# Kernel optimization log

Measured on AMD Instinct MI355X. Metric: run time of the kernel, lower is better.

The kernel has to match this reference:

```python
import jax, jax.numpy as jnp
import numpy as np

WS = 7
C = 384
NH = 12
HD = C // NH
HID = 4 * C


def layernorm(x, g, b, eps=1e-5):
    m = jnp.mean(x, axis=-1, keepdims=True)
    v = jnp.mean((x - m) ** 2, axis=-1, keepdims=True)
    return (x - m) * jax.lax.rsqrt(v + eps) * g + b


def setup_inputs() -> dict:
    key = jax.random.key(0)
    ks = jax.random.split(key, 12)
    s = 0.02
    return {
        "tokens": jax.random.normal(ks[0], (2, 8, 56 * 56, C), jnp.float32),
        "in_proj_w": jax.random.normal(ks[1], (3 * C, C), jnp.float32) * s,
        "in_proj_b": jnp.zeros((3 * C,), jnp.float32),
        "out_w": jax.random.normal(ks[2], (C, C), jnp.float32) * s,
        "out_b": jnp.zeros((C,), jnp.float32),
        "ln1_g": jnp.ones((C,), jnp.float32),
        "ln1_b": jnp.zeros((C,), jnp.float32),
        "w1": jax.random.normal(ks[3], (HID, C), jnp.float32) * s,
        "b1": jnp.zeros((HID,), jnp.float32),
        "w2": jax.random.normal(ks[4], (C, HID), jnp.float32) * s,
        "b2": jnp.zeros((C,), jnp.float32),
        "ln2_g": jnp.ones((C,), jnp.float32),
        "ln2_b": jnp.zeros((C,), jnp.float32),
        "h": 56,
        "w": 56,
    }


def _block(tokens, in_proj_w, in_proj_b, out_w, out_b, ln1_g, ln1_b, w1, b1, w2, b2, ln2_g, ln2_b, h, w):
    b, t, _, c = tokens.shape
    orig_h, orig_w = h, w
    x = tokens.reshape(b, t, h, w, c)
    pad_h = (-h) % WS
    pad_w = (-w) % WS
    if pad_h > 0 or pad_w > 0:
        x = jnp.pad(x, ((0, 0), (0, 0), (0, pad_h), (0, pad_w), (0, 0)))
        h, w = h + pad_h, w + pad_w
    nh, nw = h // WS, w // WS
    # window partition -> [N, 49, C]
    x = x.reshape(b, t, nh, WS, nw, WS, c).transpose(0, 1, 2, 4, 3, 5, 6)
    win = x.reshape(b * t * nh * nw, WS * WS, c)
    # MHA (torch nn.MultiheadAttention semantics)
    a = layernorm(win, ln1_g, ln1_b)
    qkv = a @ in_proj_w.T + in_proj_b  # [N, 49, 3C]
    q, k, v = jnp.split(qkv, 3, axis=-1)
    n, s, _ = q.shape
    q = q.reshape(n, s, NH, HD).transpose(0, 2, 1, 3)
    k = k.reshape(n, s, NH, HD).transpose(0, 2, 1, 3)
    v = v.reshape(n, s, NH, HD).transpose(0, 2, 1, 3)
    scores = jnp.einsum("nhqd,nhkd->nhqk", q, k) / jnp.sqrt(jnp.asarray(HD, q.dtype))
    p = jax.nn.softmax(scores, axis=-1)
    o = jnp.einsum("nhqk,nhkd->nhqd", p, v).transpose(0, 2, 1, 3).reshape(n, s, c)
    win = win + (o @ out_w.T + out_b)
    # MLP
    m = layernorm(win, ln2_g, ln2_b)
    m = jax.nn.gelu(m @ w1.T + b1, approximate=False) @ w2.T + b2
    win = win + m
    # window reverse
    x = win.reshape(b, t, nh, nw, WS, WS, c).transpose(0, 1, 2, 4, 3, 5, 6).reshape(b, t, h, w, c)
    x = x[:, :, :orig_h, :orig_w, :]
    return x.reshape(b, t, orig_h * orig_w, c)


def reference(tokens, in_proj_w, in_proj_b, out_w, out_b, ln1_g, ln1_b, w1, b1, w2, b2, ln2_g, ln2_b, h, w):
    return _block(tokens, in_proj_w, in_proj_b, out_w, out_b, ln1_g, ln1_b, w1, b1, w2, b2, ln2_g, ln2_b, h, w)
```

## Files before the change

### kernel.cpp

```cpp
#include <hip/hip_runtime.h>
#include <hip/hip_bf16.h>
#include <math.h>

using short8 = __attribute__((ext_vector_type(8))) short;
using f32x4  = __attribute__((ext_vector_type(4))) float;

#define MFMA_B16(A,B,C) __builtin_amdgcn_mfma_f32_16x16x32_bf16((A),(B),(C),0,0,0)

#define ALN_STR 392
#define ALN_SZ  38416
#define POOL    76832
#define PS      34816
#define QK_STR  72
#define VT_STR  72
#define OH_STR  72
#define HID_STR 136
#define SMEM_BYTES 146464

__device__ __forceinline__ unsigned short f2bfu(float x) {
  unsigned u = __float_as_uint(x);
  return (unsigned short)((u + 0x7fffu + ((u >> 16) & 1u)) >> 16);
}
__device__ __forceinline__ unsigned pk2(float a, float b) {
  return (unsigned)f2bfu(a) | ((unsigned)f2bfu(b) << 16);
}

template<bool WBF>
__device__ __forceinline__ short8 loadW(const void* base, int tile, int K8, int kcb,
                                        int l, int row, int ldk, int k0) {
  if constexpr (WBF) {
    return *(const short8*)((const unsigned short*)base +
                            (((size_t)(tile * K8 + kcb)) << 7) + l * 8);
  } else {
    const float* p = (const float*)base + (size_t)row * ldk + k0;
    float4 x = *(const float4*)p;
    float4 y = *(const float4*)(p + 4);
    short8 r;
    r[0]=(short)f2bfu(x.x); r[1]=(short)f2bfu(x.y); r[2]=(short)f2bfu(x.z); r[3]=(short)f2bfu(x.w);
    r[4]=(short)f2bfu(y.x); r[5]=(short)f2bfu(y.y); r[6]=(short)f2bfu(y.z); r[7]=(short)f2bfu(y.w);
    return r;
  }
}

__global__ void cvt_pack(const float* __restrict__ src, unsigned short* __restrict__ dst,
                         int K, int n) {
  int K8 = K >> 3;
  int i = blockIdx.x * blockDim.x + threadIdx.x;
  if (i >= n) return;
  int e = i & 7;
  int idx = i >> 3;
  int r = idx & 15; idx >>= 4;
  int kc = idx % K8, ci = idx / K8;
  dst[i] = f2bfu(src[(size_t)(ci * 16 + r) * K + kc * 8 + e]);
}

template<bool WBF>
__global__ __launch_bounds__(1024, 4)
void swin_mfma(const float* __restrict__ tokens,
               const void* __restrict__ ipw,  const float* __restrict__ ipb,
               const void* __restrict__ outw, const float* __restrict__ outb,
               const float* __restrict__ ln1g, const float* __restrict__ ln1b,
               const void* __restrict__ w1,   const float* __restrict__ b1,
               const void* __restrict__ w2,   const float* __restrict__ b2,
               const float* __restrict__ ln2g, const float* __restrict__ ln2b,
               float* __restrict__ out)
{
  extern __shared__ char smem[];
  const int tid = threadIdx.x;
  const int win = tid >> 9;
  const int wv  = (tid >> 6) & 7;
  const int l   = tid & 63;
  const int cl  = l & 15, kg = l >> 4;
  const int wid = blockIdx.x * 2 + win;
  const int iw = wid & 7, ih = (wid >> 3) & 7, bt = wid >> 6;

  unsigned short* aln = (unsigned short*)(smem + win * ALN_SZ);
  char* pool = smem + POOL + win * PS;
  unsigned short* q2   = (unsigned short*)(pool);
  unsigned short* k2   = (unsigned short*)(pool + 7056);
  unsigned short* vT2  = (unsigned short*)(pool + 14112);
  unsigned short* oh   = (unsigned short*)(pool + 23328);
  unsigned short* hid0 = (unsigned short*)(pool);
  unsigned short* hid1 = (unsigned short*)(pool + 17408);

  auto gidx = [&](int r, int c) -> size_t {
    int wi = r / 7, wj = r - wi * 7;
    return ((size_t)bt * 3136 + (size_t)((ih*7 + wi) * 56 + iw*7 + wj)) * 384 + c;
  };

  auto ln_pass = [&](const float* src, const float* gw, const float* gb) {
    int row = (tid >> 3) & 63, lj = tid & 7;
    if (row < 49) {
      size_t base = gidx(row, 0);
      float4 xv[12];
      float sx = 0.f, sxx = 0.f;
      #pragma unroll
      for (int k = 0; k < 12; ++k) {
        xv[k] = *(const float4*)&src[base + (lj + 8*k) * 4];
        sx  += xv[k].x + xv[k].y + xv[k].z + xv[k].w;
        sxx += xv[k].x*xv[k].x + xv[k].y*xv[k].y + xv[k].z*xv[k].z + xv[k].w*xv[k].w;
      }
      #pragma unroll
      for (int d = 1; d < 8; d <<= 1) { sx += __shfl_xor(sx, d, 8); sxx += __shfl_xor(sxx, d, 8); }
      float mean = sx * (1.f/384.f);
      float rs = rsqrtf(sxx * (1.f/384.f) - mean*mean + 1e-5f);
      unsigned short* arow = aln + row * ALN_STR;
      #pragma unroll
      for (int k = 0; k < 12; ++k) {
        int c = (lj + 8*k) * 4;
        float4 gv = *(const float4*)&gw[c];
        float4 bv = *(const float4*)&gb[c];
        unsigned u0 = pk2((xv[k].x-mean)*rs*gv.x + bv.x, (xv[k].y-mean)*rs*gv.y + bv.y);
        unsigned u1 = pk2((xv[k].z-mean)*rs*gv.z + bv.z, (xv[k].w-mean)*rs*gv.w + bv.w);
        *(uint2*)&arow[c] = make_uint2(u0, u1);
      }
    }
  };

  const int ri0 = wv & 3, chalf = wv >> 2;
  const int arow0 = (cl + 16 * ri0) * ALN_STR;

  auto qkv = [&](int pr) {
    #pragma unroll
    for (int half = 0; half < 2; ++half) {
      int tilea[3], growa[3], parta[3], wta[3];
      #pragma unroll
      for (int j = 0; j < 3; ++j) {
        int ci = chalf + 2 * (half * 3 + j);
        parta[j] = ci >> 2; wta[j] = ci & 3;
        tilea[j] = parta[j] * 24 + pr * 4 + wta[j];
        growa[j] = parta[j] * 384 + pr * 64 + wta[j] * 16 + cl;
      }
      f32x4 d0{0,0,0,0}, d1{0,0,0,0}, d2{0,0,0,0};
      short8 a_c  = *(const short8*)&aln[arow0 + kg*8];
      short8 b0_c = loadW<WBF>(ipw, tilea[0], 48, 0, l, growa[0], 384, kg*8);
      short8 b1_c = loadW<WBF>(ipw, tilea[1], 48, 0, l, growa[1], 384, kg*8);
      short8 b2_c = loadW<WBF>(ipw, tilea[2], 48, 0, l, growa[2], 384, kg*8);
      #pragma unroll
      for (int kt = 0; kt < 12; ++kt) {
        short8 a_n, b0_n, b1_n, b2_n;
        if (kt < 11) {
          int k1 = (kt+1)*32 + kg*8;
          a_n  = *(const short8*)&aln[arow0 + k1];
          b0_n = loadW<WBF>(ipw, tilea[0], 48, (kt+1)*4, l, growa[0], 384, k1);
          b1_n = loadW<WBF>(ipw, tilea[1], 48, (kt+1)*4, l, growa[1], 384, k1);
          b2_n = loadW<WBF>(ipw, tilea[2], 48, (kt+1)*4, l, growa[2], 384, k1);
        }
        d0 = MFMA_B16(a_c, b0_c, d0);
        d1 = MFMA_B16(a_c, b1_c, d1);
        d2 = MFMA_B16(a_c, b2_c, d2);
        a_c = a_n; b0_c = b0_n; b1_c = b1_n; b2_c = b2_n;
      }
      #pragma unroll
      for (int j = 0; j < 3; ++j) {
        f32x4 dd = (j == 0) ? d0 : (j == 1) ? d1 : d2;
        int within = wta[j] * 16 + cl;
        float bias = ipb[growa[j]];
        float scl = (parta[j] == 0) ? 0.17677669529663687f : 1.f;
        #pragma unroll
        for (int rg = 0; rg < 4; ++rg) {
          int row = kg * 4 + rg + 16 * ri0;
          if (row < 49) {
            unsigned short bv = f2bfu((dd[rg] + bias) * scl);
            if      (parta[j] == 0) q2[row * QK_STR + within] = bv;
            else if (parta[j] == 1) k2[row * QK_STR + within] = bv;
            else                    vT2[within * VT_STR + row] = bv;
          }
        }
      }
    }
  };

  for (int i = (tid & 511); i < (64*VT_STR)/2; i += 512)
    ((unsigned*)(pool + 14112))[i] = 0u;
  ln_pass(tokens, ln1g, ln1b);
  __syncthreads();

  f32x4 opacc[3][4];
  #pragma unroll
  for (int a = 0; a < 3; ++a)
    #pragma unroll
    for (int b = 0; b < 4; ++b) opacc[a][b] = f32x4{0.f,0.f,0.f,0.f};

  qkv(0);
  __syncthreads();

  const int hl = wv & 1, qci = wv >> 1;

  for (int pr = 0; pr < 6; ++pr) {
    {
      short8 bq = *(const short8*)&q2[(16*qci + cl) * QK_STR + hl*32 + kg*8];
      f32x4 dsc[4];
      #pragma unroll
      for (int kri = 0; kri < 4; ++kri) {
        short8 ak = *(const short8*)&k2[(16*kri + cl) * QK_STR + hl*32 + kg*8];
        f32x4 z{0.f,0.f,0.f,0.f};
        dsc[kri] = MFMA_B16(ak, bq, z);
      }
      float ev[4][4];
      float mx = -1e30f;
      #pragma unroll
      for (int kri = 0; kri < 4; ++kri)
        #pragma unroll
        for (int r = 0; r < 4; ++r) {
          int kidx = 16*kri + 4*kg + r;
          float v = (kidx < 49) ? dsc[kri][r] : -1e30f;
          ev[kri][r] = v;
          mx = fmaxf(mx, v);
        }
      mx = fmaxf(mx, __shfl_xor(mx, 16));
      mx = fmaxf(mx, __shfl_xor(mx, 32));
      float sum = 0.f;
      #pragma unroll
      for (int kri = 0; kri < 4; ++kri)
        #pragma unroll
        for (int r = 0; r < 4; ++r) {
          float e = __expf(ev[kri][r] - mx);
          ev[kri][r] = e; sum += e;
        }
      sum += __shfl_xor(sum, 16);
      sum += __shfl_xor(sum, 32);
      float inv = 1.f / sum;
      unsigned pk[4][2];
      #pragma unroll
      for (int kri = 0; kri < 4; ++kri) {
        pk[kri][0] = pk2(ev[kri][0]*inv, ev[kri][1]*inv);
        pk[kri][1] = pk2(ev[kri][2]*inv, ev[kri][3]*inv);
      }
      f32x4 dot0{0.f,0.f,0.f,0.f}, dot1{0.f,0.f,0.f,0.f};
      const int sA = cl + 32 * (kg & 1);
      const bool hi = (kg >> 1) & 1;
      #pragma unroll
      for (int kt = 0; kt < 2; ++kt) {
        unsigned x0 = (unsigned)__shfl((int)pk[2*kt][0],   sA);
        unsigned x1 = (unsigned)__shfl((int)pk[2*kt][1],   sA);
        unsigned x2 = (unsigned)__shfl((int)pk[2*kt][0],   sA + 16);
        unsigned x3 = (unsigned)__shfl((int)pk[2*kt][1],   sA + 16);
        unsigned y0 = (unsigned)__shfl((int)pk[2*kt+1][0], sA);
        unsigned y1 = (unsigned)__shfl((int)pk[2*kt+1][1], sA);
        unsigned y2 = (unsigned)__shfl((int)pk[2*kt+1][0], sA + 16);
        unsigned y3 = (unsigned)__shfl((int)pk[2*kt+1][1], sA + 16);
        uint4 bu = make_uint4(hi ? y0 : x0, hi ? y1 : x1, hi ? y2 : x2, hi ? y3 : x3);
        short8 bfrag = *(short8*)&bu;
        short8 a0 = *(const short8*)&vT2[(hl*32 +  0 + cl) * VT_STR + kt*32 + kg*8];
        short8 a1 = *(const short8*)&vT2[(hl*32 + 16 + cl) * VT_STR + kt*32 + kg*8];
        dot0 = MFMA_B16(a0, bfrag, dot0);
        dot1 = MFMA_B16(a1, bfrag, dot1);
      }
      int q = 16*qci + cl;
      if (q < 49) {
        int base = q * OH_STR + hl*32 + kg*4;
        *(unsigned*)&oh[base     ] = pk2(dot0[0], dot0[1]);
        *(unsigned*)&oh[base +  2] = pk2(dot0[2], dot0[3]);
        *(unsigned*)&oh[base + 16] = pk2(dot1[0], dot1[1]);
        *(unsigned*)&oh[base + 18] = pk2(dot1[2], dot1[3]);
      }
    }
    __syncthreads();

    {
      short8 ao[4][2];
      #pragma unroll
      for (int ri = 0; ri < 4; ++ri)
        #pragma unroll
        for (int kt = 0; kt < 2; ++kt)
          ao[ri][kt] = *(const short8*)&oh[(cl + 16*ri) * OH_STR + kt*32 + kg*8];
      #pragma unroll
      for (int cii = 0; cii < 3; ++cii) {
        #pragma unroll
        for (int kt = 0; kt < 2; ++kt) {
          short8 bw = loadW<WBF>(outw, wv*3 + cii, 48, pr*8 + kt*4, l,
                                 (wv*3 + cii)*16 + cl, 384, pr*64 + kt*32 + kg*8);
          opacc[cii][0] = MFMA_B16(ao[0][kt], bw, opacc[cii][0]);
          opacc[cii][1] = MFMA_B16(ao[1][kt], bw, opacc[cii][1]);
          opacc[cii][2] = MFMA_B16(ao[2][kt], bw, opacc[cii][2]);
          opacc[cii][3] = MFMA_B16(ao[3][kt], bw, opacc[cii][3]);
        }
      }
      if (pr < 5) qkv(pr + 1);
    }
    __syncthreads();
  }

  #pragma unroll
  for (int cii = 0; cii < 3; ++cii) {
    int col = (wv*3 + cii) * 16 + cl;
    float ob = outb[col];
    #pragma unroll
    for (int ri = 0; ri < 4; ++ri) {
      #pragma unroll
      for (int rg = 0; rg < 4; ++rg) {
        int row = kg*4 + rg + 16*ri;
        if (row < 49) {
          size_t g = gidx(row, col);
          out[g] = tokens[g] + opacc[cii][ri][rg] + ob;
        }
      }
    }
  }
  __syncthreads();

  ln_pass(out, ln2g, ln2b);
  __syncthreads();

  f32x4 macc[3][4];
  #pragma unroll
  for (int a = 0; a < 3; ++a)
    #pragma unroll
    for (int b = 0; b < 4; ++b) macc[a][b] = f32x4{0.f,0.f,0.f,0.f};

  auto mlp1 = [&](int cc, unsigned short* hb) {
    int tile = cc * 8 + wv;
    int n = cc * 128 + wv * 16 + cl;
    f32x4 e0{0,0,0,0}, e1{0,0,0,0}, e2{0,0,0,0}, e3{0,0,0,0};
    short8 bw_c = loadW<WBF>(w1, tile, 48, 0, l, n, 384, kg*8);
    #pragma unroll
    for (int kt = 0; kt < 12; ++kt) {
      short8 bw_n;
      if (kt < 11)
        bw_n = loadW<WBF>(w1, tile, 48, (kt+1)*4, l, n, 384, (kt+1)*32 + kg*8);
      int k0 = kt * 32 + kg * 8;
      short8 a0 = *(const short8*)&aln[(cl     ) * ALN_STR + k0];
      short8 a1 = *(const short8*)&aln[(cl + 16) * ALN_STR + k0];
      short8 a2 = *(const short8*)&aln[(cl + 32) * ALN_STR + k0];
      short8 a3 = *(const short8*)&aln[(cl + 48) * ALN_STR + k0];
      e0 = MFMA_B16(a0, bw_c, e0);
      e1 = MFMA_B16(a1, bw_c, e1);
      e2 = MFMA_B16(a2, bw_c, e2);
      e3 = MFMA_B16(a3, bw_c, e3);
      bw_c = bw_n;
    }
    float bb = b1[n];
    #pragma unroll
    for (int ri = 0; ri < 4; ++ri) {
      f32x4 ee = (ri == 0) ? e0 : (ri == 1) ? e1 : (ri == 2) ? e2 : e3;
      #pragma unroll
      for (int rg = 0; rg < 4; ++rg) {
        int row = kg*4 + rg + 16*ri;
        if (row < 49) {
          float x = ee[rg] + bb;
          float t2 = 0.044715f * x * x;
          float arg = __builtin_fmaf(t2, x, x);
          float e = __expf(1.5957691216f * arg);
          float gl = x * (e / (e + 1.f));
          hb[row * HID_STR + wv*16 + cl] = f2bfu(gl);
        }
      }
    }
  };
  auto mlp2 = [&](int cc, const unsigned short* hb) {
    short8 c0_c = loadW<WBF>(w2, wv*3+0, 192, cc*16, l, (wv*3+0)*16+cl, 1536, cc*128 + kg*8);
    short8 c1_c = loadW<WBF>(w2, wv*3+1, 192, cc*16, l, (wv*3+1)*16+cl, 1536, cc*128 + kg*8);
    short8 c2_c = loadW<WBF>(w2, wv*3+2, 192, cc*16, l, (wv*3+2)*16+cl, 1536, cc*128 + kg*8);
    #pragma unroll
    for (int kt = 0; kt < 4; ++kt) {
      short8 c0_n, c1_n, c2_n;
      if (kt < 3) {
        int kcb = cc*16 + (kt+1)*4, k1 = cc*128 + (kt+1)*32 + kg*8;
        c0_n = loadW<WBF>(w2, wv*3+0, 192, kcb, l, (wv*3+0)*16+cl, 1536, k1);
        c1_n = loadW<WBF>(w2, wv*3+1, 192, kcb, l, (wv*3+1)*16+cl, 1536, k1);
        c2_n = loadW<WBF>(w2, wv*3+2, 192, kcb, l, (wv*3+2)*16+cl, 1536, k1);
      }
      int k0 = kt * 32 + kg * 8;
      short8 h0_ = *(const short8*)&hb[(cl     ) * HID_STR + k0];
      short8 h1_ = *(const short8*)&hb[(cl + 16) * HID_STR + k0];
      short8 h2_ = *(const short8*)&hb[(cl + 32) * HID_STR + k0];
      short8 h3_ = *(const short8*)&hb[(cl + 48) * HID_STR + k0];
      macc[0][0] = MFMA_B16(h0_, c0_c, macc[0][0]);
      macc[0][1] = MFMA_B16(h1_, c0_c, macc[0][1]);
      macc[0][2] = MFMA_B16(h2_, c0_c, macc[0][2]);
      macc[0][3] = MFMA_B16(h3_, c0_c, macc[0][3]);
      macc[1][0] = MFMA_B16(h0_, c1_c, macc[1][0]);
      macc[1][1] = MFMA_B16(h1_, c1_c, macc[1][1]);
      macc[1][2] = MFMA_B16(h2_, c1_c, macc[1][2]);
      macc[1][3] = MFMA_B16(h3_, c1_c, macc[1][3]);
      macc[2][0] = MFMA_B16(h0_, c2_c, macc[2][0]);
      macc[2][1] = MFMA_B16(h1_, c2_c, macc[2][1]);
      macc[2][2] = MFMA_B16(h2_, c2_c, macc[2][2]);
      macc[2][3] = MFMA_B16(h3_, c2_c, macc[2][3]);
      c0_c = c0_n; c1_c = c1_n; c2_c = c2_n;
    }
  };

  mlp1(0, hid0);
  __syncthreads();
  for (int cc = 1; cc < 12; ++cc) {
    mlp2(cc - 1, ((cc - 1) & 1) ? hid1 : hid0);
    mlp1(cc, (cc & 1) ? hid1 : hid0);
    __syncthreads();
  }
  mlp2(11, hid1);

  #pragma unroll
  for (int cii = 0; cii < 3; ++cii) {
    int col = (wv*3 + cii) * 16 + cl;
    float bb2 = b2[col];
    #pragma unroll
    for (int ri = 0; ri < 4; ++ri) {
      #pragma unroll
      for (int rg = 0; rg < 4; ++rg) {
        int row = kg*4 + rg + 16*ri;
        if (row < 49) {
          size_t g = gidx(row, col);
          out[g] = out[g] + macc[cii][ri][rg] + bb2;
        }
      }
    }
  }
}

#define WS_IPW  0
#define WS_OUTW 442368
#define WS_W1   589824
#define WS_W2   1179648
#define WS_TOT  1769472

extern "C" void kernel_launch(void* const* d_in, const int* in_sizes, int n_in,
                              void* d_out, int out_size, void* d_ws, size_t ws_size,
                              hipStream_t stream) {
  (void)in_sizes; (void)n_in; (void)out_size;
  const float* tokens = (const float*)d_in[0];
  const float* ipw  = (const float*)d_in[1];
  const float* ipb  = (const float*)d_in[2];
  const float* outw = (const float*)d_in[3];
  const float* outb = (const float*)d_in[4];
  const float* ln1g = (const float*)d_in[5];
  const float* ln1b = (const float*)d_in[6];
  const float* w1   = (const float*)d_in[7];
  const float* b1   = (const float*)d_in[8];
  const float* w2   = (const float*)d_in[9];
  const float* b2   = (const float*)d_in[10];
  const float* ln2g = (const float*)d_in[11];
  const float* ln2b = (const float*)d_in[12];
  float* out = (float*)d_out;

  bool wbf = (ws_size >= (size_t)WS_TOT * 2);
  if (wbf) {
    unsigned short* wsp = (unsigned short*)d_ws;
    hipLaunchKernelGGL(cvt_pack, dim3((442368+511)/512), dim3(512), 0, stream, ipw,  wsp + WS_IPW,  384,  442368);
    hipLaunchKernelGGL(cvt_pack, dim3((147456+511)/512), dim3(512), 0, stream, outw, wsp + WS_OUTW, 384,  147456);
    hipLaunchKernelGGL(cvt_pack, dim3((589824+511)/512), dim3(512), 0, stream, w1,   wsp + WS_W1,   384,  589824);
    hipLaunchKernelGGL(cvt_pack, dim3((589824+511)/512), dim3(512), 0, stream, w2,   wsp + WS_W2,   1536, 589824);
    (void)hipFuncSetAttribute((const void*)swin_mfma<true>,
                              hipFuncAttributeMaxDynamicSharedMemorySize, SMEM_BYTES);
    hipLaunchKernelGGL((swin_mfma<true>), dim3(512), dim3(1024), SMEM_BYTES, stream,
                       tokens, (const void*)(wsp + WS_IPW), ipb,
                       (const void*)(wsp + WS_OUTW), outb, ln1g, ln1b,
                       (const void*)(wsp + WS_W1), b1, (const void*)(wsp + WS_W2), b2,
                       ln2g, ln2b, out);
  } else {
    (void)hipFuncSetAttribute((const void*)swin_mfma<false>,
                              hipFuncAttributeMaxDynamicSharedMemorySize, SMEM_BYTES);
    hipLaunchKernelGGL((swin_mfma<false>), dim3(512), dim3(1024), SMEM_BYTES, stream,
                       tokens, (const void*)ipw, ipb, (const void*)outw, outb, ln1g, ln1b,
                       (const void*)w1, b1, (const void*)w2, b2, ln2g, ln2b, out);
  }
}
```

Before: 501.2 us.

## Repartition MFMA warp tiling to row-block by column-half for out-proj and MLP

Changes the per-wave work split in the out-projection and both MLP GEMMs. Previously each wave covered all four 16-row blocks for a few output columns; now each wave owns one row block and half of the columns. The LN2 activation fragments for its row block are kept in registers (alnA), which removes repeated LDS reads in MLP1. The manual software prefetch of weights in the QKV and MLP loops is dropped in favour of straight loads. The trade-off is more weight fragment loads per wave, since each wave now loads four times as many distinct weight tiles, and higher register pressure from alnA.

```diff
diff --git a/kernel.cpp b/kernel.cpp
--- a/kernel.cpp
+++ b/kernel.cpp
@@ -117,8 +117,9 @@
     }
   };
 
-  const int ri0 = wv & 3, chalf = wv >> 2;
-  const int arow0 = (cl + 16 * ri0) * ALN_STR;
+  const int ri = wv & 3;
+  const int ch = wv >> 2;
+  const int arow0 = (cl + 16 * ri) * ALN_STR;
 
   auto qkv = [&](int pr) {
     #pragma unroll
@@ -126,30 +127,22 @@
       int tilea[3], growa[3], parta[3], wta[3];
       #pragma unroll
       for (int j = 0; j < 3; ++j) {
-        int ci = chalf + 2 * (half * 3 + j);
+        int ci = ch + 2 * (half * 3 + j);
         parta[j] = ci >> 2; wta[j] = ci & 3;
         tilea[j] = parta[j] * 24 + pr * 4 + wta[j];
         growa[j] = parta[j] * 384 + pr * 64 + wta[j] * 16 + cl;
       }
       f32x4 d0{0,0,0,0}, d1{0,0,0,0}, d2{0,0,0,0};
-      short8 a_c  = *(const short8*)&aln[arow0 + kg*8];
-      short8 b0_c = loadW<WBF>(ipw, tilea[0], 48, 0, l, growa[0], 384, kg*8);
-      short8 b1_c = loadW<WBF>(ipw, tilea[1], 48, 0, l, growa[1], 384, kg*8);
-      short8 b2_c = loadW<WBF>(ipw, tilea[2], 48, 0, l, growa[2], 384, kg*8);
       #pragma unroll
       for (int kt = 0; kt < 12; ++kt) {
-        short8 a_n, b0_n, b1_n, b2_n;
-        if (kt < 11) {
-          int k1 = (kt+1)*32 + kg*8;
-          a_n  = *(const short8*)&aln[arow0 + k1];
-          b0_n = loadW<WBF>(ipw, tilea[0], 48, (kt+1)*4, l, growa[0], 384, k1);
-          b1_n = loadW<WBF>(ipw, tilea[1], 48, (kt+1)*4, l, growa[1], 384, k1);
-          b2_n = loadW<WBF>(ipw, tilea[2], 48, (kt+1)*4, l, growa[2], 384, k1);
-        }
-        d0 = MFMA_B16(a_c, b0_c, d0);
-        d1 = MFMA_B16(a_c, b1_c, d1);
-        d2 = MFMA_B16(a_c, b2_c, d2);
-        a_c = a_n; b0_c = b0_n; b1_c = b1_n; b2_c = b2_n;
+        int k0 = kt * 32 + kg * 8;
+        short8 a  = *(const short8*)&aln[arow0 + k0];
+        short8 b0 = loadW<WBF>(ipw, tilea[0], 48, kt*4, l, growa[0], 384, k0);
+        short8 bb1 = loadW<WBF>(ipw, tilea[1], 48, kt*4, l, growa[1], 384, k0);
+        short8 bb2 = loadW<WBF>(ipw, tilea[2], 48, kt*4, l, growa[2], 384, k0);
+        d0 = MFMA_B16(a, b0, d0);
+        d1 = MFMA_B16(a, bb1, d1);
+        d2 = MFMA_B16(a, bb2, d2);
       }
       #pragma unroll
       for (int j = 0; j < 3; ++j) {
@@ -159,7 +152,7 @@
         float scl = (parta[j] == 0) ? 0.17677669529663687f : 1.f;
         #pragma unroll
         for (int rg = 0; rg < 4; ++rg) {
-          int row = kg * 4 + rg + 16 * ri0;
+          int row = kg * 4 + rg + 16 * ri;
           if (row < 49) {
             unsigned short bv = f2bfu((dd[rg] + bias) * scl);
             if      (parta[j] == 0) q2[row * QK_STR + within] = bv;
@@ -176,11 +169,9 @@
   ln_pass(tokens, ln1g, ln1b);
   __syncthreads();
 
-  f32x4 opacc[3][4];
+  f32x4 opacc[12];
   #pragma unroll
-  for (int a = 0; a < 3; ++a)
-    #pragma unroll
-    for (int b = 0; b < 4; ++b) opacc[a][b] = f32x4{0.f,0.f,0.f,0.f};
+  for (int j = 0; j < 12; ++j) opacc[j] = f32x4{0.f,0.f,0.f,0.f};
 
   qkv(0);
   __syncthreads();
@@ -259,23 +250,15 @@
     __syncthreads();
 
     {
-      short8 ao[4][2];
-      #pragma unroll
-      for (int ri = 0; ri < 4; ++ri)
-        #pragma unroll
-        for (int kt = 0; kt < 2; ++kt)
-          ao[ri][kt] = *(const short8*)&oh[(cl + 16*ri) * OH_STR + kt*32 + kg*8];
-      #pragma unroll
-      for (int cii = 0; cii < 3; ++cii) {
-        #pragma unroll
-        for (int kt = 0; kt < 2; ++kt) {
-          short8 bw = loadW<WBF>(outw, wv*3 + cii, 48, pr*8 + kt*4, l,
-                                 (wv*3 + cii)*16 + cl, 384, pr*64 + kt*32 + kg*8);
-          opacc[cii][0] = MFMA_B16(ao[0][kt], bw, opacc[cii][0]);
-          opacc[cii][1] = MFMA_B16(ao[1][kt], bw, opacc[cii][1]);
-          opacc[cii][2] = MFMA_B16(ao[2][kt], bw, opacc[cii][2]);
-          opacc[cii][3] = MFMA_B16(ao[3][kt], bw, opacc[cii][3]);
-        }
+      short8 ao0 = *(const short8*)&oh[(cl + 16*ri) * OH_STR +      kg*8];
+      short8 ao1 = *(const short8*)&oh[(cl + 16*ri) * OH_STR + 32 + kg*8];
+      #pragma unroll
+      for (int j = 0; j < 12; ++j) {
+        int ct = ch*12 + j;
+        short8 bw0 = loadW<WBF>(outw, ct, 48, pr*8,     l, ct*16 + cl, 384, pr*64      + kg*8);
+        short8 bw1 = loadW<WBF>(outw, ct, 48, pr*8 + 4, l, ct*16 + cl, 384, pr*64 + 32 + kg*8);
+        opacc[j] = MFMA_B16(ao0, bw0, opacc[j]);
+        opacc[j] = MFMA_B16(ao1, bw1, opacc[j]);
       }
       if (pr < 5) qkv(pr + 1);
     }
@@ -283,18 +266,15 @@
   }
 
   #pragma unroll
-  for (int cii = 0; cii < 3; ++cii) {
-    int col = (wv*3 + cii) * 16 + cl;
+  for (int j = 0; j < 12; ++j) {
+    int col = (ch*12 + j) * 16 + cl;
     float ob = outb[col];
     #pragma unroll
-    for (int ri = 0; ri < 4; ++ri) {
-      #pragma unroll
-      for (int rg = 0; rg < 4; ++rg) {
-        int row = kg*4 + rg + 16*ri;
-        if (row < 49) {
-          size_t g = gidx(row, col);
-          out[g] = tokens[g] + opacc[cii][ri][rg] + ob;
-        }
+    for (int rg = 0; rg < 4; ++rg) {
+      int row = 16*ri + kg*4 + rg;
+      if (row < 49) {
+        size_t g = gidx(row, col);
+        out[g] = tokens[g] + opacc[j][rg] + ob;
       }
     }
   }
@@ -303,82 +283,59 @@
   ln_pass(out, ln2g, ln2b);
   __syncthreads();
 
-  f32x4 macc[3][4];
+  short8 alnA[12];
   #pragma unroll
-  for (int a = 0; a < 3; ++a)
-    #pragma unroll
-    for (int b = 0; b < 4; ++b) macc[a][b] = f32x4{0.f,0.f,0.f,0.f};
+  for (int kt = 0; kt < 12; ++kt)
+    alnA[kt] = *(const short8*)&aln[arow0 + kt*32 + kg*8];
+
+  f32x4 macc[12];
+  #pragma unroll
+  for (int j = 0; j < 12; ++j) macc[j] = f32x4{0.f,0.f,0.f,0.f};
 
   auto mlp1 = [&](int cc, unsigned short* hb) {
-    int tile = cc * 8 + wv;
-    int n = cc * 128 + wv * 16 + cl;
     f32x4 e0{0,0,0,0}, e1{0,0,0,0}, e2{0,0,0,0}, e3{0,0,0,0};
-    short8 bw_c = loadW<WBF>(w1, tile, 48, 0, l, n, 384, kg*8);
     #pragma unroll
     for (int kt = 0; kt < 12; ++kt) {
-      short8 bw_n;
-      if (kt < 11)
-        bw_n = loadW<WBF>(w1, tile, 48, (kt+1)*4, l, n, 384, (kt+1)*32 + kg*8);
-      int k0 = kt * 32 + kg * 8;
-      short8 a0 = *(const short8*)&aln[(cl     ) * ALN_STR + k0];
-      short8 a1 = *(const short8*)&aln[(cl + 16) * ALN_STR + k0];
-      short8 a2 = *(const short8*)&aln[(cl + 32) * ALN_STR + k0];
-      short8 a3 = *(const short8*)&aln[(cl + 48) * ALN_STR + k0];
-      e0 = MFMA_B16(a0, bw_c, e0);
-      e1 = MFMA_B16(a1, bw_c, e1);
-      e2 = MFMA_B16(a2, bw_c, e2);
-      e3 = MFMA_B16(a3, bw_c, e3);
-      bw_c = bw_n;
-    }
-    float bb = b1[n];
-    #pragma unroll
-    for (int ri = 0; ri < 4; ++ri) {
-      f32x4 ee = (ri == 0) ? e0 : (ri == 1) ? e1 : (ri == 2) ? e2 : e3;
+      int k0 = kt*32 + kg*8;
+      short8 wb0 = loadW<WBF>(w1, cc*8 + ch*4 + 0, 48, kt*4, l, (cc*8+ch*4+0)*16 + cl, 384, k0);
+      short8 wb1 = loadW<WBF>(w1, cc*8 + ch*4 + 1, 48, kt*4, l, (cc*8+ch*4+1)*16 + cl, 384, k0);
+      short8 wb2 = loadW<WBF>(w1, cc*8 + ch*4 + 2, 48, kt*4, l, (cc*8+ch*4+2)*16 + cl, 384, k0);
+      short8 wb3 = loadW<WBF>(w1, cc*8 + ch*4 + 3, 48, kt*4, l, (cc*8+ch*4+3)*16 + cl, 384, k0);
+      e0 = MFMA_B16(alnA[kt], wb0, e0);
+      e1 = MFMA_B16(alnA[kt], wb1, e1);
+      e2 = MFMA_B16(alnA[kt], wb2, e2);
+      e3 = MFMA_B16(alnA[kt], wb3, e3);
+    }
+    #pragma unroll
+    for (int j = 0; j < 4; ++j) {
+      f32x4 ee = (j == 0) ? e0 : (j == 1) ? e1 : (j == 2) ? e2 : e3;
+      int n = cc*128 + ch*64 + j*16 + cl;
+      float bb = b1[n];
       #pragma unroll
       for (int rg = 0; rg < 4; ++rg) {
-        int row = kg*4 + rg + 16*ri;
+        int row = 16*ri + kg*4 + rg;
         if (row < 49) {
           float x = ee[rg] + bb;
           float t2 = 0.044715f * x * x;
           float arg = __builtin_fmaf(t2, x, x);
           float e = __expf(1.5957691216f * arg);
           float gl = x * (e / (e + 1.f));
-          hb[row * HID_STR + wv*16 + cl] = f2bfu(gl);
+          hb[row * HID_STR + ch*64 + j*16 + cl] = f2bfu(gl);
         }
       }
     }
   };
   auto mlp2 = [&](int cc, const unsigned short* hb) {
-    short8 c0_c = loadW<WBF>(w2, wv*3+0, 192, cc*16, l, (wv*3+0)*16+cl, 1536, cc*128 + kg*8);
-    short8 c1_c = loadW<WBF>(w2, wv*3+1, 192, cc*16, l, (wv*3+1)*16+cl, 1536, cc*128 + kg*8);
-    short8 c2_c = loadW<WBF>(w2, wv*3+2, 192, cc*16, l, (wv*3+2)*16+cl, 1536, cc*128 + kg*8);
     #pragma unroll
     for (int kt = 0; kt < 4; ++kt) {
-      short8 c0_n, c1_n, c2_n;
-      if (kt < 3) {
-        int kcb = cc*16 + (kt+1)*4, k1 = cc*128 + (kt+1)*32 + kg*8;
-        c0_n = loadW<WBF>(w2, wv*3+0, 192, kcb, l, (wv*3+0)*16+cl, 1536, k1);
-        c1_n = loadW<WBF>(w2, wv*3+1, 192, kcb, l, (wv*3+1)*16+cl, 1536, k1);
-        c2_n = loadW<WBF>(w2, wv*3+2, 192, kcb, l, (wv*3+2)*16+cl, 1536, k1);
-      }
-      int k0 = kt * 32 + kg * 8;
-      short8 h0_ = *(const short8*)&hb[(cl     ) * HID_STR + k0];
-      short8 h1_ = *(const short8*)&hb[(cl + 16) * HID_STR + k0];
-      short8 h2_ = *(const short8*)&hb[(cl + 32) * HID_STR + k0];
-      short8 h3_ = *(const short8*)&hb[(cl + 48) * HID_STR + k0];
-      macc[0][0] = MFMA_B16(h0_, c0_c, macc[0][0]);
-      macc[0][1] = MFMA_B16(h1_, c0_c, macc[0][1]);
-      macc[0][2] = MFMA_B16(h2_, c0_c, macc[0][2]);
-      macc[0][3] = MFMA_B16(h3_, c0_c, macc[0][3]);
-      macc[1][0] = MFMA_B16(h0_, c1_c, macc[1][0]);
-      macc[1][1] = MFMA_B16(h1_, c1_c, macc[1][1]);
-      macc[1][2] = MFMA_B16(h2_, c1_c, macc[1][2]);
-      macc[1][3] = MFMA_B16(h3_, c1_c, macc[1][3]);
-      macc[2][0] = MFMA_B16(h0_, c2_c, macc[2][0]);
-      macc[2][1] = MFMA_B16(h1_, c2_c, macc[2][1]);
-      macc[2][2] = MFMA_B16(h2_, c2_c, macc[2][2]);
-      macc[2][3] = MFMA_B16(h3_, c2_c, macc[2][3]);
-      c0_c = c0_n; c1_c = c1_n; c2_c = c2_n;
+      short8 hd = *(const short8*)&hb[(cl + 16*ri) * HID_STR + kt*32 + kg*8];
+      #pragma unroll
+      for (int j = 0; j < 12; ++j) {
+        int ct = ch*12 + j;
+        short8 bw = loadW<WBF>(w2, ct, 192, cc*16 + kt*4, l,
+                               ct*16 + cl, 1536, cc*128 + kt*32 + kg*8);
+        macc[j] = MFMA_B16(hd, bw, macc[j]);
+      }
     }
   };
 
@@ -392,18 +349,15 @@
   mlp2(11, hid1);
 
   #pragma unroll
-  for (int cii = 0; cii < 3; ++cii) {
-    int col = (wv*3 + cii) * 16 + cl;
+  for (int j = 0; j < 12; ++j) {
+    int col = (ch*12 + j) * 16 + cl;
     float bb2 = b2[col];
     #pragma unroll
-    for (int ri = 0; ri < 4; ++ri) {
-      #pragma unroll
-      for (int rg = 0; rg < 4; ++rg) {
-        int row = kg*4 + rg + 16*ri;
-        if (row < 49) {
-          size_t g = gidx(row, col);
-          out[g] = out[g] + macc[cii][ri][rg] + bb2;
-        }
+    for (int rg = 0; rg < 4; ++rg) {
+      int row = 16*ri + kg*4 + rg;
+      if (row < 49) {
+        size_t g = gidx(row, col);
+        out[g] = out[g] + macc[j][rg] + bb2;
       }
     }
   }
```

Result: slower. 954.7 us (+90.5%).
